# Kernel tuning notes

Hardware: AMD Instinct MI355X
Metric: run time of the kernel (lower is better)

## Reference

```python
import jax, jax.numpy as jnp
import numpy as np

B, D = 16384, 1280      # batch, EfficientNet-b0 feature dim (model._fc.in_features)
C1, C2, C3 = 8, 6, 4    # fanout per tree level: 8 roots, 6 children each, 4 leaves each


def setup_inputs() -> dict:
    key = jax.random.key(0)
    ks = jax.random.split(key, 7)
    sc = 0.02
    x = jax.random.normal(ks[0], (B, D), dtype=jnp.float32)
    # root classifier: self.final = Linear(1280 -> n[0]=8)
    W_final = jax.random.normal(ks[1], (D, C1), dtype=jnp.float32) * sc
    b_final = jnp.zeros((C1,), dtype=jnp.float32)
    # level-1 node linears: Linear(1281 -> 6); split into feature part Wp and upper-scalar column wu
    Wp1 = jax.random.normal(ks[2], (C1, D, C2), dtype=jnp.float32) * sc
    wu1 = jax.random.normal(ks[3], (C1, C2), dtype=jnp.float32) * sc
    b1 = jnp.zeros((C1, C2), dtype=jnp.float32)
    # level-2 node linears: Linear(1281 -> 4)
    Wp2 = jax.random.normal(ks[4], (C1, C2, D, C3), dtype=jnp.float32) * sc
    wu2 = jax.random.normal(ks[5], (C1, C2, C3), dtype=jnp.float32) * sc
    b2 = jnp.zeros((C1, C2, C3), dtype=jnp.float32)
    return {"x": x, "W_final": W_final, "b_final": b_final,
            "Wp1": Wp1, "wu1": wu1, "b1": b1,
            "Wp2": Wp2, "wu2": wu2, "b2": b2}


def reference(x, W_final, b_final, Wp1, wu1, b1, Wp2, wu2, b2):
    # penultimate = x.clone().detach()
    pen = jax.lax.stop_gradient(x)                      # (B, D)
    # root: raw final-linear outputs (NO softmax at root in the torch code)
    u1 = x @ W_final + b_final                          # (B, C1) == upper for level-1 nodes
    # level-1 nodes: line = softmax(Linear([pen, upper_scalar]))
    # Linear([pen, u]) == pen @ Wp + u * wu + b  (batched over all 8 nodes in one GEMM)
    logits1 = jnp.einsum('bd,idc->bic', pen, Wp1) + u1[:, :, None] * wu1[None] + b1[None]
    p1 = jax.nn.softmax(logits1, axis=-1)               # (B, C1, C2)
    u2 = p1 * u1[:, :, None]                            # upper for level-2 nodes
    # level-2 nodes
    logits2 = jnp.einsum('bd,ijdc->bijc', pen, Wp2) + u2[..., None] * wu2[None] + b2[None]
    p2 = jax.nn.softmax(logits2, axis=-1)               # (B, C1, C2, C3)
    u3 = p2 * u2[..., None]                             # upper for leaf nodes
    # output: for each node (sorted by path length, then lexicographic path),
    # the last column of xdict[node] == upper[node]. Row-major reshape matches
    # the sorted key order for single-char labels.
    return jnp.concatenate([u1, u2.reshape(B, C1 * C2), u3.reshape(B, C1 * C2 * C3)], axis=1)
```

## Files before the change

kernel.cpp:

```cpp
#include <hip/hip_runtime.h>
#include <stdint.h>
#include <stddef.h>

#define D_FEAT 1280
#define N_PAD  256
#define N_OUT  248
#define BM     64
#define BK     64
#define K_ITERS 20
#define W_TILE_BYTES (N_PAD * BK * 2)
#define A_TILE_BYTES (BM * BK * 4)

typedef float f32x4 __attribute__((ext_vector_type(4)));
typedef short s16x8 __attribute__((ext_vector_type(8)));
typedef unsigned int u32x4 __attribute__((ext_vector_type(4)));

__device__ __forceinline__ unsigned short f2bf(float f) {
  union { float f; unsigned int u; } v; v.f = f;
  unsigned int r = (v.u + 0x7fffu + ((v.u >> 16) & 1u)) >> 16;
  return (unsigned short)r;
}

__device__ __forceinline__ unsigned int cvt_pk(float a, float b) {
  unsigned int r;
  asm("v_cvt_pk_bf16_f32 %0, %1, %2" : "=v"(r) : "v"(a), "v"(b));
  return r;
}

__device__ __forceinline__ void gload16(const void* g, void* l) {
  __builtin_amdgcn_global_load_lds(
      (const __attribute__((address_space(1))) void*)g,
      (__attribute__((address_space(3))) void*)l, 16, 0, 0);
}

__global__ __launch_bounds__(256) void pack_w_kernel(
    const float* __restrict__ Wf, const float* __restrict__ Wp1,
    const float* __restrict__ Wp2, unsigned short* __restrict__ out) {
  int idx = blockIdx.x * 256 + threadIdx.x;
  int e = idx & 7;
  int chunk = idx >> 3;
  int s_phys = chunk & 7;
  int n = (chunk >> 3) & 255;
  int kt = chunk >> 11;
  int s_log = s_phys ^ (n & 7);
  int d = kt * BK + s_log * 8 + e;
  float v = 0.0f;
  if (n < 8) {
    v = Wf[d * 8 + n];
  } else if (n < 56) {
    int m = n - 8;
    v = Wp1[((m / 6) * D_FEAT + d) * 6 + (m % 6)];
  } else if (n < 248) {
    int m = n - 56;
    v = Wp2[(((m / 24) * 6 + ((m % 24) >> 2)) * D_FEAT + d) * 4 + (m & 3)];
  }
  out[idx] = f2bf(v);
}

__global__ __launch_bounds__(512, 2) void tree_head_kernel(
    const float* __restrict__ x, const unsigned short* __restrict__ Wb,
    const float* __restrict__ b_final, const float* __restrict__ wu1,
    const float* __restrict__ b1, const float* __restrict__ wu2,
    const float* __restrict__ b2, float* __restrict__ out) {
  __shared__ __align__(16) char smem[147456];
  char* A0 = smem;
  char* A1 = smem + 16384;
  char* A2 = smem + 32768;
  char* B0 = smem + 49152;
  char* B1 = smem + 81920;
  char* B2 = smem + 114688;

  const int tid  = threadIdx.x;
  const int lane = tid & 63;
  const int wave = tid >> 6;
  const int wm   = wave >> 2;
  const int wn   = wave & 3;
  const int l15  = lane & 15;
  const int lh   = lane >> 4;
  const int row0 = blockIdx.x * BM;

  f32x4 acc[2][4];
#pragma unroll
  for (int m = 0; m < 2; ++m)
#pragma unroll
    for (int n = 0; n < 4; ++n)
#pragma unroll
      for (int j = 0; j < 4; ++j) acc[m][n][j] = 0.0f;

  const char* asrc[2];
  int adst[2];
#pragma unroll
  for (int j = 0; j < 2; ++j) {
    int q = wave * 2 + j;
    int rl = 4 * q + lh;
    asrc[j] = (const char*)x + (size_t)(row0 + rl) * (D_FEAT * 4)
              + ((l15 ^ (rl & 15)) << 4);
    adst[j] = q * 1024;
  }
  const char* bsrc = (const char*)Wb + wave * 4096 + lane * 16;
  const int bdst = wave * 4096;

#define STAGE(kt_, dA, dB) do {                                               \
    _Pragma("unroll")                                                         \
    for (int j_ = 0; j_ < 4; ++j_)                                            \
      gload16(bsrc + (size_t)(kt_) * W_TILE_BYTES + j_ * 1024,                \
              (dB) + bdst + j_ * 1024);                                       \
    _Pragma("unroll")                                                         \
    for (int j_ = 0; j_ < 2; ++j_)                                            \
      gload16(asrc[j_] + (kt_) * 256, (dA) + adst[j_]);                       \
  } while (0)

#define COMPUTE(cA, cB) do {                                                  \
    s16x8 fr[2][2];                                                           \
    _Pragma("unroll")                                                         \
    for (int m_ = 0; m_ < 2; ++m_) {                                          \
      int rl_ = wm * 32 + m_ * 16 + l15;                                      \
      const char* rb_ = (cA) + rl_ * 256;                                     \
      _Pragma("unroll")                                                       \
      for (int ks_ = 0; ks_ < 2; ++ks_) {                                     \
        int s0_ = ks_ * 8 + lh * 2;                                           \
        f32x4 f0_ = *(const f32x4*)(rb_ + ((s0_ ^ (rl_ & 15)) << 4));         \
        f32x4 f1_ = *(const f32x4*)(rb_ + (((s0_ + 1) ^ (rl_ & 15)) << 4));   \
        union { u32x4 u; s16x8 s; } pk_;                                      \
        pk_.u[0] = cvt_pk(f0_[0], f0_[1]); pk_.u[1] = cvt_pk(f0_[2], f0_[3]); \
        pk_.u[2] = cvt_pk(f1_[0], f1_[1]); pk_.u[3] = cvt_pk(f1_[2], f1_[3]); \
        fr[m_][ks_] = pk_.s;                                                  \
      }                                                                       \
    }                                                                         \
    _Pragma("unroll")                                                         \
    for (int ks_ = 0; ks_ < 2; ++ks_) {                                       \
      int sl_ = ks_ * 4 + lh;                                                 \
      _Pragma("unroll")                                                       \
      for (int nf_ = 0; nf_ < 4; ++nf_) {                                     \
        int n_ = wn * 64 + nf_ * 16 + l15;                                    \
        s16x8 b_ = *(const s16x8*)((cB) + n_ * 128 + ((sl_ ^ (n_ & 7)) << 4));\
        acc[0][nf_] = __builtin_amdgcn_mfma_f32_16x16x32_bf16(fr[0][ks_], b_, acc[0][nf_], 0, 0, 0); \
        acc[1][nf_] = __builtin_amdgcn_mfma_f32_16x16x32_bf16(fr[1][ks_], b_, acc[1][nf_], 0, 0, 0); \
      }                                                                       \
    }                                                                         \
  } while (0)

#define ITER_MAIN(kt_, cA, cB, nA, nB) do {                                   \
    asm volatile("s_waitcnt vmcnt(6)" ::: "memory");                          \
    __builtin_amdgcn_sched_barrier(0);                                        \
    __builtin_amdgcn_s_barrier();                                             \
    __builtin_amdgcn_sched_barrier(0);                                        \
    STAGE((kt_) + 2, nA, nB);                                                 \
    __builtin_amdgcn_sched_barrier(0);                                        \
    COMPUTE(cA, cB);                                                          \
  } while (0)

  STAGE(0, A0, B0);
  STAGE(1, A1, B1);

  for (int t = 0; t < 6; ++t) {
    int kt = 3 * t;
    ITER_MAIN(kt,     A0, B0, A2, B2);
    ITER_MAIN(kt + 1, A1, B1, A0, B0);
    ITER_MAIN(kt + 2, A2, B2, A1, B1);
  }

  asm volatile("s_waitcnt vmcnt(6)" ::: "memory");
  __builtin_amdgcn_sched_barrier(0);
  __builtin_amdgcn_s_barrier();
  __builtin_amdgcn_sched_barrier(0);
  COMPUTE(A0, B0);

  asm volatile("s_waitcnt vmcnt(0)" ::: "memory");
  __builtin_amdgcn_sched_barrier(0);
  __builtin_amdgcn_s_barrier();
  __builtin_amdgcn_sched_barrier(0);
  COMPUTE(A1, B1);

  __syncthreads();

  float* Ls = (float*)smem;
#pragma unroll
  for (int m = 0; m < 2; ++m)
#pragma unroll
    for (int nf = 0; nf < 4; ++nf) {
      int col = wn * 64 + nf * 16 + l15;
      if (col < N_OUT) {
        int rbase = wm * 32 + m * 16 + (lh << 2);
#pragma unroll
        for (int i = 0; i < 4; ++i) Ls[col * 65 + rbase + i] = acc[m][nf][i];
      }
    }
  __syncthreads();

  const int p = tid & 7;
  const int r = tid >> 3;
  float* orow = out + (size_t)(row0 + r) * N_OUT;

  float ui = Ls[p * 65 + r] + b_final[p];
  orow[p] = ui;

  float lg[6];
  float mx = -1e30f;
#pragma unroll
  for (int c = 0; c < 6; ++c) {
    lg[c] = Ls[(8 + p * 6 + c) * 65 + r] + ui * wu1[p * 6 + c] + b1[p * 6 + c];
    mx = fmaxf(mx, lg[c]);
  }
  float s = 0.0f;
#pragma unroll
  for (int c = 0; c < 6; ++c) { lg[c] = __expf(lg[c] - mx); s += lg[c]; }
  float sc = ui / s;
  float u2v[6];
#pragma unroll
  for (int c = 0; c < 6; ++c) {
    u2v[c] = lg[c] * sc;
    orow[8 + p * 6 + c] = u2v[c];
  }

#pragma unroll
  for (int j = 0; j < 6; ++j) {
    int g = p * 6 + j;
    float ug = u2v[j];
    float l2[4];
    float m2 = -1e30f;
#pragma unroll
    for (int c = 0; c < 4; ++c) {
      l2[c] = Ls[(56 + g * 4 + c) * 65 + r] + ug * wu2[g * 4 + c] + b2[g * 4 + c];
      m2 = fmaxf(m2, l2[c]);
    }
    float s2 = 0.0f;
#pragma unroll
    for (int c = 0; c < 4; ++c) { l2[c] = __expf(l2[c] - m2); s2 += l2[c]; }
    float sc2 = ug / s2;
    f32x4 o;
#pragma unroll
    for (int c = 0; c < 4; ++c) o[c] = l2[c] * sc2;
    *(f32x4*)(orow + 56 + g * 4) = o;
  }
#undef STAGE
#undef COMPUTE
#undef ITER_MAIN
}

extern "C" void kernel_launch(void* const* d_in, const int* in_sizes, int n_in,
                              void* d_out, int out_size, void* d_ws, size_t ws_size,
                              hipStream_t stream) {
  const float* x   = (const float*)d_in[0];
  const float* Wf  = (const float*)d_in[1];
  const float* bf  = (const float*)d_in[2];
  const float* Wp1 = (const float*)d_in[3];
  const float* wu1 = (const float*)d_in[4];
  const float* b1  = (const float*)d_in[5];
  const float* Wp2 = (const float*)d_in[6];
  const float* wu2 = (const float*)d_in[7];
  const float* b2  = (const float*)d_in[8];
  float* out = (float*)d_out;
  unsigned short* Wb = (unsigned short*)d_ws;

  pack_w_kernel<<<1280, 256, 0, stream>>>(Wf, Wp1, Wp2, Wb);
  tree_head_kernel<<<16384 / BM, 512, 0, stream>>>(x, Wb, bf, wu1, b1, wu2, b2, out);
}
```

Measured before the change: 33.36 us.

## Convert x to bf16 in registers before LDS, shrinking A tiles and pipeline

The A operand was previously copied straight from global to LDS as fp32 and converted to bf16 by every wave at compute time. It is now loaded into registers two iterations ahead, converted once per element, and written to LDS as bf16. This halves the A-tile footprint (LDS drops from 144KB to 120KB) and removes redundant conversions across the four N-waves. The cost is added register pressure from the staging buffers and an extra lgkmcnt wait plus LDS write on the critical path each iteration.

```diff
diff --git a/kernel.cpp b/kernel.cpp
--- a/kernel.cpp
+++ b/kernel.cpp
@@ -9,7 +9,6 @@
 #define BK     64
 #define K_ITERS 20
 #define W_TILE_BYTES (N_PAD * BK * 2)
-#define A_TILE_BYTES (BM * BK * 4)
 
 typedef float f32x4 __attribute__((ext_vector_type(4)));
 typedef short s16x8 __attribute__((ext_vector_type(8)));
@@ -62,13 +61,13 @@
     const float* __restrict__ b_final, const float* __restrict__ wu1,
     const float* __restrict__ b1, const float* __restrict__ wu2,
     const float* __restrict__ b2, float* __restrict__ out) {
-  __shared__ __align__(16) char smem[147456];
+  __shared__ __align__(16) char smem[122880];
   char* A0 = smem;
-  char* A1 = smem + 16384;
-  char* A2 = smem + 32768;
-  char* B0 = smem + 49152;
-  char* B1 = smem + 81920;
-  char* B2 = smem + 114688;
+  char* A1 = smem + 8192;
+  char* A2 = smem + 16384;
+  char* B0 = smem + 24576;
+  char* B1 = smem + 57344;
+  char* B2 = smem + 90112;
 
   const int tid  = threadIdx.x;
   const int lane = tid & 63;
@@ -87,44 +86,46 @@
 #pragma unroll
       for (int j = 0; j < 4; ++j) acc[m][n][j] = 0.0f;
 
-  const char* asrc[2];
-  int adst[2];
-#pragma unroll
-  for (int j = 0; j < 2; ++j) {
-    int q = wave * 2 + j;
-    int rl = 4 * q + lh;
-    asrc[j] = (const char*)x + (size_t)(row0 + rl) * (D_FEAT * 4)
-              + ((l15 ^ (rl & 15)) << 4);
-    adst[j] = q * 1024;
-  }
-  const char* bsrc = (const char*)Wb + wave * 4096 + lane * 16;
-  const int bdst = wave * 4096;
-
-#define STAGE(kt_, dA, dB) do {                                               \
+  const int arow = tid >> 3;
+  const int aslot = tid & 7;
+  const char* aptr = (const char*)x + ((size_t)(row0 + arow) * D_FEAT + aslot * 8) * 4;
+  const int awoff = arow * 128 + ((aslot ^ (arow & 7)) << 4);
+  const char* bsrc = (const char*)Wb + wave * 1024 + lane * 16;
+  const int bdst = wave * 1024;
+
+  f32x4 ra[3][2];
+
+#define STAGEB(kt_, dB_) do {                                                 \
     _Pragma("unroll")                                                         \
     for (int j_ = 0; j_ < 4; ++j_)                                            \
-      gload16(bsrc + (size_t)(kt_) * W_TILE_BYTES + j_ * 1024,                \
-              (dB) + bdst + j_ * 1024);                                       \
-    _Pragma("unroll")                                                         \
-    for (int j_ = 0; j_ < 2; ++j_)                                            \
-      gload16(asrc[j_] + (kt_) * 256, (dA) + adst[j_]);                       \
-  } while (0)
-
-#define COMPUTE(cA, cB) do {                                                  \
+      gload16(bsrc + (size_t)(kt_) * W_TILE_BYTES + j_ * 8192,                \
+              (dB_) + bdst + j_ * 8192);                                      \
+  } while (0)
+
+#define LOADA(kt_, ri_) do {                                                  \
+    ra[ri_][0] = *(const f32x4*)(aptr + (kt_) * 256);                         \
+    ra[ri_][1] = *(const f32x4*)(aptr + (kt_) * 256 + 16);                    \
+  } while (0)
+
+#define WRITEA(ri_, dA_) do {                                                 \
+    union { u32x4 u; s16x8 s; } pk_;                                          \
+    pk_.u[0] = cvt_pk(ra[ri_][0][0], ra[ri_][0][1]);                          \
+    pk_.u[1] = cvt_pk(ra[ri_][0][2], ra[ri_][0][3]);                          \
+    pk_.u[2] = cvt_pk(ra[ri_][1][0], ra[ri_][1][1]);                          \
+    pk_.u[3] = cvt_pk(ra[ri_][1][2], ra[ri_][1][3]);                          \
+    *(s16x8*)((dA_) + awoff) = pk_.s;                                         \
+  } while (0)
+
+#define COMPUTE(cA_, cB_) do {                                                \
     s16x8 fr[2][2];                                                           \
     _Pragma("unroll")                                                         \
     for (int m_ = 0; m_ < 2; ++m_) {                                          \
       int rl_ = wm * 32 + m_ * 16 + l15;                                      \
-      const char* rb_ = (cA) + rl_ * 256;                                     \
       _Pragma("unroll")                                                       \
       for (int ks_ = 0; ks_ < 2; ++ks_) {                                     \
-        int s0_ = ks_ * 8 + lh * 2;                                           \
-        f32x4 f0_ = *(const f32x4*)(rb_ + ((s0_ ^ (rl_ & 15)) << 4));         \
-        f32x4 f1_ = *(const f32x4*)(rb_ + (((s0_ + 1) ^ (rl_ & 15)) << 4));   \
-        union { u32x4 u; s16x8 s; } pk_;                                      \
-        pk_.u[0] = cvt_pk(f0_[0], f0_[1]); pk_.u[1] = cvt_pk(f0_[2], f0_[3]); \
-        pk_.u[2] = cvt_pk(f1_[0], f1_[1]); pk_.u[3] = cvt_pk(f1_[2], f1_[3]); \
-        fr[m_][ks_] = pk_.s;                                                  \
+        int sl_ = ks_ * 4 + lh;                                               \
+        fr[m_][ks_] = *(const s16x8*)((cA_) + rl_ * 128 +                     \
+                                      ((sl_ ^ (rl_ & 7)) << 4));              \
       }                                                                       \
     }                                                                         \
     _Pragma("unroll")                                                         \
@@ -133,40 +134,52 @@
       _Pragma("unroll")                                                       \
       for (int nf_ = 0; nf_ < 4; ++nf_) {                                     \
         int n_ = wn * 64 + nf_ * 16 + l15;                                    \
-        s16x8 b_ = *(const s16x8*)((cB) + n_ * 128 + ((sl_ ^ (n_ & 7)) << 4));\
+        s16x8 b_ = *(const s16x8*)((cB_) + n_ * 128 + ((sl_ ^ (n_ & 7)) << 4));\
         acc[0][nf_] = __builtin_amdgcn_mfma_f32_16x16x32_bf16(fr[0][ks_], b_, acc[0][nf_], 0, 0, 0); \
         acc[1][nf_] = __builtin_amdgcn_mfma_f32_16x16x32_bf16(fr[1][ks_], b_, acc[1][nf_], 0, 0, 0); \
       }                                                                       \
     }                                                                         \
   } while (0)
 
-#define ITER_MAIN(kt_, cA, cB, nA, nB) do {                                   \
+#define ITER(kt_, cA_, cB_, wA_, sB_, rl_, rc_) do {                          \
+    asm volatile("s_waitcnt lgkmcnt(0)" ::: "memory");                        \
+    __builtin_amdgcn_sched_barrier(0);                                        \
+    __builtin_amdgcn_s_barrier();                                             \
+    __builtin_amdgcn_sched_barrier(0);                                        \
+    STAGEB((kt_) + 2, sB_);                                                   \
+    LOADA((kt_) + 2, rl_);                                                    \
+    __builtin_amdgcn_sched_barrier(0);                                        \
     asm volatile("s_waitcnt vmcnt(6)" ::: "memory");                          \
     __builtin_amdgcn_sched_barrier(0);                                        \
-    __builtin_amdgcn_s_barrier();                                             \
-    __builtin_amdgcn_sched_barrier(0);                                        \
-    STAGE((kt_) + 2, nA, nB);                                                 \
-    __builtin_amdgcn_sched_barrier(0);                                        \
-    COMPUTE(cA, cB);                                                          \
-  } while (0)
-
-  STAGE(0, A0, B0);
-  STAGE(1, A1, B1);
+    WRITEA(rc_, wA_);                                                         \
+    COMPUTE(cA_, cB_);                                                        \
+  } while (0)
+
+  STAGEB(0, B0);
+  LOADA(0, 0);
+  STAGEB(1, B1);
+  LOADA(1, 1);
+  __builtin_amdgcn_sched_barrier(0);
+  asm volatile("s_waitcnt vmcnt(6)" ::: "memory");
+  __builtin_amdgcn_sched_barrier(0);
+  WRITEA(0, A0);
 
   for (int t = 0; t < 6; ++t) {
-    int kt = 3 * t;
-    ITER_MAIN(kt,     A0, B0, A2, B2);
-    ITER_MAIN(kt + 1, A1, B1, A0, B0);
-    ITER_MAIN(kt + 2, A2, B2, A1, B1);
-  }
-
-  asm volatile("s_waitcnt vmcnt(6)" ::: "memory");
+    ITER(3 * t + 0, A0, B0, A1, B2, 2, 1);
+    ITER(3 * t + 1, A1, B1, A2, B0, 0, 2);
+    ITER(3 * t + 2, A2, B2, A0, B1, 1, 0);
+  }
+
+  asm volatile("s_waitcnt lgkmcnt(0)" ::: "memory");
   __builtin_amdgcn_sched_barrier(0);
   __builtin_amdgcn_s_barrier();
   __builtin_amdgcn_sched_barrier(0);
+  asm volatile("s_waitcnt vmcnt(0)" ::: "memory");
+  __builtin_amdgcn_sched_barrier(0);
+  WRITEA(1, A1);
   COMPUTE(A0, B0);
 
-  asm volatile("s_waitcnt vmcnt(0)" ::: "memory");
+  asm volatile("s_waitcnt lgkmcnt(0)" ::: "memory");
   __builtin_amdgcn_sched_barrier(0);
   __builtin_amdgcn_s_barrier();
   __builtin_amdgcn_sched_barrier(0);
@@ -233,9 +246,11 @@
     for (int c = 0; c < 4; ++c) o[c] = l2[c] * sc2;
     *(f32x4*)(orow + 56 + g * 4) = o;
   }
-#undef STAGE
+#undef STAGEB
+#undef LOADA
+#undef WRITEA
 #undef COMPUTE
-#undef ITER_MAIN
+#undef ITER
 }
 
 extern "C" void kernel_launch(void* const* d_in, const int* in_sizes, int n_in,
```

New measurement: 35.86 us. +7.5%, slower.
